# Optimization experiments

Hardware: AMD Instinct MI355X
Metric: run time of the kernel (lower is better)

## Reference

```python
import jax, jax.numpy as jnp
import numpy as np

D_MODEL = 1024
N_HEADS = 16
D_K = D_MODEL // N_HEADS
D_FF = 4096
B, S = 4, 2048
EPS = 1e-5


def setup_inputs() -> dict:
    key = jax.random.key(0)
    ks = jax.random.split(key, 16)
    s = 0.02
    inp = {
        'x': jax.random.normal(ks[0], (B, S, D_MODEL), dtype=jnp.float32),
        'Wq': jax.random.normal(ks[1], (D_MODEL, D_MODEL), dtype=jnp.float32) * s,
        'bq': jnp.zeros((D_MODEL,), jnp.float32),
        'Wk': jax.random.normal(ks[2], (D_MODEL, D_MODEL), dtype=jnp.float32) * s,
        'bk': jnp.zeros((D_MODEL,), jnp.float32),
        'Wv': jax.random.normal(ks[3], (D_MODEL, D_MODEL), dtype=jnp.float32) * s,
        'bv': jnp.zeros((D_MODEL,), jnp.float32),
        'Wo': jax.random.normal(ks[4], (D_MODEL, D_MODEL), dtype=jnp.float32) * s,
        'bo': jnp.zeros((D_MODEL,), jnp.float32),
        'W1': jax.random.normal(ks[5], (D_MODEL, D_FF), dtype=jnp.float32) * s,
        'b1': jnp.zeros((D_FF,), jnp.float32),
        'W2': jax.random.normal(ks[6], (D_FF, D_MODEL), dtype=jnp.float32) * s,
        'b2': jnp.zeros((D_MODEL,), jnp.float32),
        'g1': jnp.ones((D_MODEL,), jnp.float32),
        'be1': jnp.zeros((D_MODEL,), jnp.float32),
        'g2': jnp.ones((D_MODEL,), jnp.float32),
        'be2': jnp.zeros((D_MODEL,), jnp.float32),
    }
    return inp


def _layernorm(x, g, b):
    mu = jnp.mean(x, axis=-1, keepdims=True)
    var = jnp.var(x, axis=-1, keepdims=True)
    return (x - mu) * jax.lax.rsqrt(var + EPS) * g + b


def reference(x, Wq, bq, Wk, bk, Wv, bv, Wo, bo, W1, b1, W2, b2, g1, be1, g2, be2):
    # Multi-head self-attention (mask=None, dropout in eval -> identity)
    q = (x @ Wq + bq).reshape(B, S, N_HEADS, D_K).transpose(0, 2, 1, 3)  # [B,H,S,Dk]
    k = (x @ Wk + bk).reshape(B, S, N_HEADS, D_K).transpose(0, 2, 1, 3)
    v = (x @ Wv + bv).reshape(B, S, N_HEADS, D_K).transpose(0, 2, 1, 3)
    scores = jnp.einsum('bhqd,bhkd->bhqk', q, k) / jnp.sqrt(jnp.float32(D_K))
    attn = jax.nn.softmax(scores, axis=-1)
    out = jnp.einsum('bhqk,bhkd->bhqd', attn, v)          # [B,H,S,Dk]
    out = out.transpose(0, 2, 1, 3).reshape(B, S, D_MODEL)
    att_out = out @ Wo + bo
    x2 = _layernorm(x + att_out, g1, be1)
    ff = jax.nn.relu(x2 @ W1 + b1) @ W2 + b2
    return _layernorm(x2 + ff, g2, be2)
```

## Files before the change

kernel.cpp:

```cpp
#include <hip/hip_runtime.h>
#include <hip/hip_bf16.h>

typedef __attribute__((ext_vector_type(8)))  __bf16 bf16x8;
typedef __attribute__((ext_vector_type(4)))  float  f32x4;
typedef __attribute__((ext_vector_type(16))) float  f32x16;

static __device__ __forceinline__ unsigned short f2bf(float x) {
    unsigned int u = __float_as_uint(x);
    unsigned int r = (u + 0x7FFFu + ((u >> 16) & 1u)) >> 16;
    return (unsigned short)r;
}
static __device__ __forceinline__ float bf2f(unsigned short u) {
    return __uint_as_float(((unsigned int)u) << 16);
}

static __device__ __forceinline__ float fast_exp2(float x) {
    float r;
    asm volatile("v_exp_f32 %0, %1\n\ts_nop 1" : "=v"(r) : "v"(x));
    return r;
}
static __device__ __forceinline__ unsigned int cvt_pk_bf16(float a, float b) {
    unsigned int r;
    asm("v_cvt_pk_bf16_f32 %0, %1, %2" : "=v"(r) : "v"(a), "v"(b));
    return r;
}

static __device__ __forceinline__ void gload_lds16(const ushort* g, ushort* l) {
    __builtin_amdgcn_global_load_lds((const __attribute__((address_space(1))) void*)g,
                                     (__attribute__((address_space(3))) void*)l, 16, 0, 0);
}

static __device__ __forceinline__ int xcd_swz(int id, int nwg) {
    return (id & 7) * (nwg >> 3) + (id >> 3);
}

__global__ __launch_bounds__(256) void cast_bf16_kernel(const float* __restrict__ in,
                                                        ushort* __restrict__ out, int n4) {
    int i = blockIdx.x * 256 + threadIdx.x;
    if (i < n4) {
        float4 v = reinterpret_cast<const float4*>(in)[i];
        ushort4 o;
        o.x = f2bf(v.x); o.y = f2bf(v.y); o.z = f2bf(v.z); o.w = f2bf(v.w);
        reinterpret_cast<ushort4*>(out)[i] = o;
    }
}

__global__ __launch_bounds__(256) void transpose_cast_kernel(const float* __restrict__ in,
                                                             ushort* __restrict__ out,
                                                             int K, int N) {
    __shared__ float tile[32][33];
    const int tx = threadIdx.x;
    const int ty = threadIdx.y;
    const int n0 = blockIdx.x * 32;
    const int k0 = blockIdx.y * 32;
    for (int i = ty; i < 32; i += 8)
        tile[i][tx] = in[(size_t)(k0 + i) * N + n0 + tx];
    __syncthreads();
    for (int i = ty; i < 32; i += 8)
        out[(size_t)(n0 + i) * K + k0 + tx] = f2bf(tile[tx][i]);
}

template<int RELU, int OUTBF, int QKV>
__global__ __launch_bounds__(256) void gemm_db(const ushort* __restrict__ A,
                                               const ushort* __restrict__ Bt,
                                               const float* __restrict__ b0,
                                               const float* __restrict__ b1_,
                                               const float* __restrict__ b2_,
                                               void* __restrict__ Cp,
                                               int M, int N, int K) {
    __shared__ ushort As[2][4096];
    __shared__ ushort Bs[2][4096];
    const int tid  = threadIdx.x;
    const int lane = tid & 63;
    const int w    = tid >> 6;
    const int wr   = w >> 1, wc = w & 1;
    const int nwg = gridDim.x * gridDim.y;
    int wid = xcd_swz(blockIdx.y * gridDim.x + blockIdx.x, nwg);
    const int bx = wid % gridDim.x;
    const int by = wid / gridDim.x;
    const int m0 = by * 128;
    const int n0 = bx * 128;
    const int lr = lane & 15;
    const int lk = (lane >> 4) * 8;

    const int r0 = w * 32 + (lane >> 2);
    const int c8 = (lane & 3) * 8;
    const ushort* gA0 = A  + (size_t)(m0 + r0)      * K + c8;
    const ushort* gA1 = A  + (size_t)(m0 + r0 + 16) * K + c8;
    const ushort* gB0 = Bt + (size_t)(n0 + r0)      * K + c8;
    const ushort* gB1 = Bt + (size_t)(n0 + r0 + 16) * K + c8;
    const int wb = w * 1024;

    f32x4 acc[4][4];
    const f32x4 z = {0.f, 0.f, 0.f, 0.f};
#pragma unroll
    for (int i = 0; i < 4; i++)
#pragma unroll
        for (int j = 0; j < 4; j++) acc[i][j] = z;

    const int nt = K >> 5;

    gload_lds16(gA0, &As[0][wb]);
    gload_lds16(gA1, &As[0][wb + 512]);
    gload_lds16(gB0, &Bs[0][wb]);
    gload_lds16(gB1, &Bs[0][wb + 512]);

    int cur = 0;
    for (int t = 0; t < nt; ++t) {
        __syncthreads();
        if (t + 1 < nt) {
            const int kn = (t + 1) * 32;
            gload_lds16(gA0 + kn, &As[cur ^ 1][wb]);
            gload_lds16(gA1 + kn, &As[cur ^ 1][wb + 512]);
            gload_lds16(gB0 + kn, &Bs[cur ^ 1][wb]);
            gload_lds16(gB1 + kn, &Bs[cur ^ 1][wb + 512]);
        }

        const ushort* Asb = As[cur];
        const ushort* Bsb = Bs[cur];
        bf16x8 af[4], bfr[4];
#pragma unroll
        for (int i = 0; i < 4; i++)
            af[i] = *reinterpret_cast<const bf16x8*>(&Asb[(wr * 64 + i * 16 + lr) * 32 + lk]);
#pragma unroll
        for (int j = 0; j < 4; j++)
            bfr[j] = *reinterpret_cast<const bf16x8*>(&Bsb[(wc * 64 + j * 16 + lr) * 32 + lk]);
#pragma unroll
        for (int i = 0; i < 4; i++)
#pragma unroll
            for (int j = 0; j < 4; j++)
                acc[i][j] = __builtin_amdgcn_mfma_f32_16x16x32_bf16(af[i], bfr[j], acc[i][j], 0, 0, 0);
        cur ^= 1;
    }

    const float* bias;
    float qscale = 1.0f;
    if (QKV) {
        bias = (n0 < 1024) ? b0 : (n0 < 2048 ? b1_ : b2_);
        if (n0 < 1024) qscale = 0.18033688f;
    } else {
        bias = b0;
    }
    const int nb = QKV ? (n0 & 1023) : n0;
    const int rbase = (lane >> 4) * 4;
#pragma unroll
    for (int i = 0; i < 4; i++) {
#pragma unroll
        for (int j = 0; j < 4; j++) {
            const int cloc = wc * 64 + j * 16 + lr;
            const float bv = bias[nb + cloc];
#pragma unroll
            for (int r = 0; r < 4; r++) {
                const int row = m0 + wr * 64 + i * 16 + rbase + r;
                float v = acc[i][j][r] + bv;
                if (RELU) v = v > 0.f ? v : 0.f;
                if (QKV)  v *= qscale;
                if (OUTBF) ((ushort*)Cp)[(size_t)row * N + n0 + cloc] = f2bf(v);
                else       ((float*)Cp)[(size_t)row * N + n0 + cloc] = v;
            }
        }
    }
}

#define ASWZ(row, col) ((row) * 64 + ((col) ^ ((((row) ^ ((row) >> 3)) & 7) << 3)))

__global__ __launch_bounds__(256, 3) void attn_kernel(const ushort* __restrict__ QKV,
                                                      ushort* __restrict__ O) {
    __shared__ ushort Ks[2][4096];
    __shared__ ushort Vt[2][4096];
    const int tid  = threadIdx.x;
    const int lane = tid & 63;
    const int w    = tid >> 6;
    const int l31  = lane & 31;
    const int hi   = lane >> 5;

    int blk = xcd_swz(blockIdx.x, gridDim.x);
    const int qb = blk & 15;
    const int h  = (blk >> 4) & 15;
    const int b  = blk >> 8;
    const int s0 = qb * 128 + w * 32;
    const size_t rowb   = (size_t)b * 2048;
    const size_t base_q = rowb * 3072 + (size_t)h * 64;
    const size_t base_k = base_q + 1024;
    const size_t base_v = base_q + 2048;
    const size_t base_o = rowb * 1024 + (size_t)h * 64;

    bf16x8 qf[4];
#pragma unroll
    for (int ks = 0; ks < 4; ks++)
        qf[ks] = *reinterpret_cast<const bf16x8*>(
            &QKV[base_q + (size_t)(s0 + l31) * 3072 + ks * 16 + 8 * hi]);

    int off8[2][4];
#pragma unroll
    for (int sub = 0; sub < 2; sub++)
#pragma unroll
        for (int ks = 0; ks < 4; ks++)
            off8[sub][ks] = ASWZ(sub * 32 + l31, ks * 16 + 8 * hi);

    const int tS  = tid >> 3;
    const int ccS = tid & 7;
    int vwoff[2][8];
#pragma unroll
    for (int i = 0; i < 2; i++)
#pragma unroll
        for (int jj = 0; jj < 8; jj++)
            vwoff[i][jj] = ASWZ(ccS * 8 + jj, tS + i * 32);
    const int t1  = tS + 32;
    const int sz0 = (tS ^ (tS >> 3)) & 7;
    const int sz1 = (t1 ^ (t1 >> 3)) & 7;
    const ushort* pK0 = QKV + base_k + (size_t)tS * 3072 + (ccS ^ sz0) * 8;
    const ushort* pK1 = QKV + base_k + (size_t)t1 * 3072 + (ccS ^ sz1) * 8;
    const ushort* pV0 = QKV + base_v + (size_t)tS * 3072 + ccS * 8;
    const ushort* pV1 = QKV + base_v + (size_t)t1 * 3072 + ccS * 8;
    const size_t step = (size_t)64 * 3072;

    gload_lds16(pK0, &Ks[0][w * 512]);
    gload_lds16(pK1, &Ks[0][2048 + w * 512]);
    {
        int4 v0 = *reinterpret_cast<const int4*>(pV0);
        int4 v1 = *reinterpret_cast<const int4*>(pV1);
        const ushort* vs0 = reinterpret_cast<const ushort*>(&v0);
        const ushort* vs1 = reinterpret_cast<const ushort*>(&v1);
#pragma unroll
        for (int jj = 0; jj < 8; jj++) Vt[0][vwoff[0][jj]] = vs0[jj];
#pragma unroll
        for (int jj = 0; jj < 8; jj++) Vt[0][vwoff[1][jj]] = vs1[jj];
    }
    pK0 += step; pK1 += step; pV0 += step; pV1 += step;
    __syncthreads();

    f32x16 oacc0, oacc1;
    for (int i = 0; i < 16; i++) { oacc0[i] = 0.f; oacc1[i] = 0.f; }
    float lacc = 0.f;
    int cur = 0;

    for (int it = 0; it < 32; ++it) {
        int4 nv0, nv1;
        if (it < 31) {
            gload_lds16(pK0, &Ks[cur ^ 1][w * 512]);
            gload_lds16(pK1, &Ks[cur ^ 1][2048 + w * 512]);
            nv0 = *reinterpret_cast<const int4*>(pV0);
            nv1 = *reinterpret_cast<const int4*>(pV1);
            pK0 += step; pK1 += step; pV0 += step; pV1 += step;
        }

        f32x16 sa0, sa1;
        for (int i = 0; i < 16; i++) { sa0[i] = 0.f; sa1[i] = 0.f; }
        __builtin_amdgcn_s_setprio(1);
#pragma unroll
        for (int ks = 0; ks < 4; ks++) {
            bf16x8 k0 = *reinterpret_cast<const bf16x8*>(&Ks[cur][off8[0][ks]]);
            sa0 = __builtin_amdgcn_mfma_f32_32x32x16_bf16(k0, qf[ks], sa0, 0, 0, 0);
        }
#pragma unroll
        for (int ks = 0; ks < 4; ks++) {
            bf16x8 k1 = *reinterpret_cast<const bf16x8*>(&Ks[cur][off8[1][ks]]);
            sa1 = __builtin_amdgcn_mfma_f32_32x32x16_bf16(k1, qf[ks], sa1, 0, 0, 0);
        }
        __builtin_amdgcn_s_setprio(0);

        unsigned pk0[8], pk1[8];
#pragma unroll
        for (int i = 0; i < 8; i++) {
            float plo = fast_exp2(sa0[2 * i]);
            float phi = fast_exp2(sa0[2 * i + 1]);
            lacc += plo + phi;
            pk0[i] = cvt_pk_bf16(plo, phi);
        }
#pragma unroll
        for (int i = 0; i < 8; i++) {
            float plo = fast_exp2(sa1[2 * i]);
            float phi = fast_exp2(sa1[2 * i + 1]);
            lacc += plo + phi;
            pk1[i] = cvt_pk_bf16(plo, phi);
        }

        __builtin_amdgcn_s_setprio(1);
#pragma unroll
        for (int ks = 0; ks < 4; ks++) {
            const int bi = 4 * (ks & 1);
            unsigned a, bb, c, d;
            if (ks < 2) { a = pk0[bi]; bb = pk0[bi + 1]; c = pk0[bi + 2]; d = pk0[bi + 3]; }
            else        { a = pk1[bi]; bb = pk1[bi + 1]; c = pk1[bi + 2]; d = pk1[bi + 3]; }
            asm("v_permlane32_swap_b32 %0, %1" : "+v"(a), "+v"(c));
            asm("v_permlane32_swap_b32 %0, %1" : "+v"(bb), "+v"(d));
            union { unsigned u[4]; bf16x8 v; } fr;
            fr.u[0] = a; fr.u[1] = bb; fr.u[2] = c; fr.u[3] = d;
            bf16x8 v0 = *reinterpret_cast<const bf16x8*>(&Vt[cur][off8[0][ks]]);
            oacc0 = __builtin_amdgcn_mfma_f32_32x32x16_bf16(fr.v, v0, oacc0, 0, 0, 0);
            bf16x8 v1 = *reinterpret_cast<const bf16x8*>(&Vt[cur][off8[1][ks]]);
            oacc1 = __builtin_amdgcn_mfma_f32_32x32x16_bf16(fr.v, v1, oacc1, 0, 0, 0);
        }
        __builtin_amdgcn_s_setprio(0);

        if (it < 31) {
            const ushort* vs0 = reinterpret_cast<const ushort*>(&nv0);
            const ushort* vs1 = reinterpret_cast<const ushort*>(&nv1);
#pragma unroll
            for (int jj = 0; jj < 8; jj++) Vt[cur ^ 1][vwoff[0][jj]] = vs0[jj];
#pragma unroll
            for (int jj = 0; jj < 8; jj++) Vt[cur ^ 1][vwoff[1][jj]] = vs1[jj];
        }
        __syncthreads();
        cur ^= 1;
    }

    const float ltot = lacc + __shfl_xor(lacc, 32);
    const float inv  = 1.f / ltot;
#pragma unroll
    for (int r = 0; r < 16; r++) {
        const int qloc = (r & 3) + 8 * (r >> 2) + 4 * hi;
        const float invq = __shfl(inv, qloc);
        const size_t rowoff = base_o + (size_t)(s0 + qloc) * 1024 + l31;
        O[rowoff]      = f2bf(oacc0[r] * invq);
        O[rowoff + 32] = f2bf(oacc1[r] * invq);
    }
}

__global__ __launch_bounds__(256) void ln_res_fb(const float* __restrict__ x,
                                                 const ushort* __restrict__ y,
                                                 const float* __restrict__ g,
                                                 const float* __restrict__ be,
                                                 ushort* __restrict__ outb) {
    const int row = blockIdx.x;
    const int tid = threadIdx.x;
    const float4 xv = reinterpret_cast<const float4*>(x + (size_t)row * 1024)[tid];
    const ushort4 yv = reinterpret_cast<const ushort4*>(y + (size_t)row * 1024)[tid];
    float v[4] = {xv.x + bf2f(yv.x), xv.y + bf2f(yv.y), xv.z + bf2f(yv.z), xv.w + bf2f(yv.w)};
    float s  = v[0] + v[1] + v[2] + v[3];
    float s2 = v[0]*v[0] + v[1]*v[1] + v[2]*v[2] + v[3]*v[3];
    for (int off = 32; off; off >>= 1) { s += __shfl_down(s, off); s2 += __shfl_down(s2, off); }
    __shared__ float red[8];
    const int w = tid >> 6, lane = tid & 63;
    if (lane == 0) { red[w] = s; red[4 + w] = s2; }
    __syncthreads();
    if (tid == 0) {
        const float ts  = red[0] + red[1] + red[2] + red[3];
        const float ts2 = red[4] + red[5] + red[6] + red[7];
        const float mu  = ts * (1.f / 1024.f);
        const float var = ts2 * (1.f / 1024.f) - mu * mu;
        red[0] = mu;
        red[1] = rsqrtf(var + 1e-5f);
    }
    __syncthreads();
    const float mu = red[0], rs = red[1];
    const float4 gv = reinterpret_cast<const float4*>(g)[tid];
    const float4 bv = reinterpret_cast<const float4*>(be)[tid];
    ushort4 ob;
    ob.x = f2bf((v[0] - mu) * rs * gv.x + bv.x);
    ob.y = f2bf((v[1] - mu) * rs * gv.y + bv.y);
    ob.z = f2bf((v[2] - mu) * rs * gv.z + bv.z);
    ob.w = f2bf((v[3] - mu) * rs * gv.w + bv.w);
    reinterpret_cast<ushort4*>(outb + (size_t)row * 1024)[tid] = ob;
}

__global__ __launch_bounds__(256) void ln_res_bb(const ushort* __restrict__ x,
                                                 const ushort* __restrict__ y,
                                                 const float* __restrict__ g,
                                                 const float* __restrict__ be,
                                                 float* __restrict__ outf) {
    const int row = blockIdx.x;
    const int tid = threadIdx.x;
    const ushort4 xv = reinterpret_cast<const ushort4*>(x + (size_t)row * 1024)[tid];
    const ushort4 yv = reinterpret_cast<const ushort4*>(y + (size_t)row * 1024)[tid];
    float v[4] = {bf2f(xv.x) + bf2f(yv.x), bf2f(xv.y) + bf2f(yv.y),
                  bf2f(xv.z) + bf2f(yv.z), bf2f(xv.w) + bf2f(yv.w)};
    float s  = v[0] + v[1] + v[2] + v[3];
    float s2 = v[0]*v[0] + v[1]*v[1] + v[2]*v[2] + v[3]*v[3];
    for (int off = 32; off; off >>= 1) { s += __shfl_down(s, off); s2 += __shfl_down(s2, off); }
    __shared__ float red[8];
    const int w = tid >> 6, lane = tid & 63;
    if (lane == 0) { red[w] = s; red[4 + w] = s2; }
    __syncthreads();
    if (tid == 0) {
        const float ts  = red[0] + red[1] + red[2] + red[3];
        const float ts2 = red[4] + red[5] + red[6] + red[7];
        const float mu  = ts * (1.f / 1024.f);
        const float var = ts2 * (1.f / 1024.f) - mu * mu;
        red[0] = mu;
        red[1] = rsqrtf(var + 1e-5f);
    }
    __syncthreads();
    const float mu = red[0], rs = red[1];
    const float4 gv = reinterpret_cast<const float4*>(g)[tid];
    const float4 bv = reinterpret_cast<const float4*>(be)[tid];
    float4 of;
    of.x = (v[0] - mu) * rs * gv.x + bv.x;
    of.y = (v[1] - mu) * rs * gv.y + bv.y;
    of.z = (v[2] - mu) * rs * gv.z + bv.z;
    of.w = (v[3] - mu) * rs * gv.w + bv.w;
    reinterpret_cast<float4*>(outf + (size_t)row * 1024)[tid] = of;
}

extern "C" void kernel_launch(void* const* d_in, const int* in_sizes, int n_in,
                              void* d_out, int out_size, void* d_ws, size_t ws_size,
                              hipStream_t stream) {
    const float* x  = (const float*)d_in[0];
    const float* Wq = (const float*)d_in[1];  const float* bq = (const float*)d_in[2];
    const float* Wk = (const float*)d_in[3];  const float* bk = (const float*)d_in[4];
    const float* Wv = (const float*)d_in[5];  const float* bv = (const float*)d_in[6];
    const float* Wo = (const float*)d_in[7];  const float* bo = (const float*)d_in[8];
    const float* W1 = (const float*)d_in[9];  const float* b1 = (const float*)d_in[10];
    const float* W2 = (const float*)d_in[11]; const float* b2 = (const float*)d_in[12];
    const float* g1 = (const float*)d_in[13]; const float* be1 = (const float*)d_in[14];
    const float* g2 = (const float*)d_in[15]; const float* be2 = (const float*)d_in[16];

    char* ws = (char*)d_ws;
    const size_t MBy = (size_t)1 << 20;
    ushort* xb    = (ushort*)(ws + 0 * MBy);
    ushort* wqkvT = (ushort*)(ws + 16 * MBy);
    ushort* woT   = (ushort*)(ws + 22 * MBy);
    ushort* w1T   = (ushort*)(ws + 24 * MBy);
    ushort* w2T   = (ushort*)(ws + 32 * MBy);
    ushort* QKVb  = (ushort*)(ws + 40 * MBy);
    ushort* AOb   = (ushort*)(ws + 88 * MBy);
    ushort* h1    = (ushort*)(ws + 40 * MBy);
    ushort* y1b   = (ushort*)(ws + 104 * MBy);
    ushort* y2b   = (ushort*)(ws + 104 * MBy);
    ushort* x2b   = (ushort*)(ws + 120 * MBy);
    (void)ws_size; (void)n_in; (void)in_sizes; (void)out_size;

    const int M = 8192;

    cast_bf16_kernel<<<(M * 1024 / 4 + 255) / 256, 256, 0, stream>>>(x, xb, M * 1024 / 4);
    dim3 tb(32, 8);
    transpose_cast_kernel<<<dim3(32, 32),  tb, 0, stream>>>(Wq, wqkvT,               1024, 1024);
    transpose_cast_kernel<<<dim3(32, 32),  tb, 0, stream>>>(Wk, wqkvT + 1024 * 1024, 1024, 1024);
    transpose_cast_kernel<<<dim3(32, 32),  tb, 0, stream>>>(Wv, wqkvT + 2048 * 1024, 1024, 1024);
    transpose_cast_kernel<<<dim3(32, 32),  tb, 0, stream>>>(Wo, woT, 1024, 1024);
    transpose_cast_kernel<<<dim3(128, 32), tb, 0, stream>>>(W1, w1T, 1024, 4096);
    transpose_cast_kernel<<<dim3(32, 128), tb, 0, stream>>>(W2, w2T, 4096, 1024);

    gemm_db<0, 1, 1><<<dim3(24, 64), 256, 0, stream>>>(xb, wqkvT, bq, bk, bv, QKVb,
                                                       M, 3072, 1024);

    attn_kernel<<<1024, 256, 0, stream>>>(QKVb, AOb);

    gemm_db<0, 1, 0><<<dim3(8, 64), 256, 0, stream>>>(AOb, woT, bo, nullptr, nullptr, y1b,
                                                      M, 1024, 1024);

    ln_res_fb<<<M, 256, 0, stream>>>(x, y1b, g1, be1, x2b);

    gemm_db<1, 1, 0><<<dim3(32, 64), 256, 0, stream>>>(x2b, w1T, b1, nullptr, nullptr, h1,
                                                       M, 4096, 1024);
    gemm_db<0, 1, 0><<<dim3(8, 64), 256, 0, stream>>>(h1, w2T, b2, nullptr, nullptr, y2b,
                                                      M, 1024, 4096);

    ln_res_bb<<<M, 256, 0, stream>>>(x2b, y2b, g2, be2, (float*)d_out);
}
```

Baseline: 430.9 us.

## Triple-buffer GEMM LDS pipeline with explicit vmcnt waits, merge QKV weight transposes

The GEMM now keeps three LDS stages and prefetches two K-tiles ahead. It replaces the blanket __syncthreads with a partial s_waitcnt vmcnt(4) plus a bare barrier, so global loads can overlap more MFMA work. The three Q/K/V weight transpose launches are also merged into one 3D-grid launch to cut launch overhead. LDS use per block rises from 32KB to 48KB, which may lower occupancy. The explicit wait counts also depend on the compiler not issuing other vector memory ops in the loop.

```diff
diff --git a/kernel.cpp b/kernel.cpp
--- a/kernel.cpp
+++ b/kernel.cpp
@@ -28,6 +28,12 @@
 static __device__ __forceinline__ void gload_lds16(const ushort* g, ushort* l) {
     __builtin_amdgcn_global_load_lds((const __attribute__((address_space(1))) void*)g,
                                      (__attribute__((address_space(3))) void*)l, 16, 0, 0);
+}
+
+static __device__ __forceinline__ void barrier_fence() {
+    __builtin_amdgcn_s_barrier();
+    __builtin_amdgcn_sched_barrier(0);
+    asm volatile("" ::: "memory");
 }
 
 static __device__ __forceinline__ int xcd_swz(int id, int nwg) {
@@ -60,16 +66,35 @@
         out[(size_t)(n0 + i) * K + k0 + tx] = f2bf(tile[tx][i]);
 }
 
+__global__ __launch_bounds__(256) void transpose_cast3_kernel(const float* __restrict__ w0,
+                                                              const float* __restrict__ w1,
+                                                              const float* __restrict__ w2,
+                                                              ushort* __restrict__ out) {
+    __shared__ float tile[32][33];
+    const int tx = threadIdx.x;
+    const int ty = threadIdx.y;
+    const int n0 = blockIdx.x * 32;
+    const int k0 = blockIdx.y * 32;
+    const int z  = blockIdx.z;
+    const float* in = (z == 0) ? w0 : (z == 1 ? w1 : w2);
+    ushort* o = out + (size_t)z * 1024 * 1024;
+    for (int i = ty; i < 32; i += 8)
+        tile[i][tx] = in[(size_t)(k0 + i) * 1024 + n0 + tx];
+    __syncthreads();
+    for (int i = ty; i < 32; i += 8)
+        o[(size_t)(n0 + i) * 1024 + k0 + tx] = f2bf(tile[tx][i]);
+}
+
 template<int RELU, int OUTBF, int QKV>
-__global__ __launch_bounds__(256) void gemm_db(const ushort* __restrict__ A,
+__global__ __launch_bounds__(256) void gemm_p3(const ushort* __restrict__ A,
                                                const ushort* __restrict__ Bt,
                                                const float* __restrict__ b0,
                                                const float* __restrict__ b1_,
                                                const float* __restrict__ b2_,
                                                void* __restrict__ Cp,
                                                int M, int N, int K) {
-    __shared__ ushort As[2][4096];
-    __shared__ ushort Bs[2][4096];
+    __shared__ ushort As[3][4096];
+    __shared__ ushort Bs[3][4096];
     const int tid  = threadIdx.x;
     const int lane = tid & 63;
     const int w    = tid >> 6;
@@ -100,20 +125,28 @@
 
     const int nt = K >> 5;
 
-    gload_lds16(gA0, &As[0][wb]);
-    gload_lds16(gA1, &As[0][wb + 512]);
-    gload_lds16(gB0, &Bs[0][wb]);
-    gload_lds16(gB1, &Bs[0][wb + 512]);
+#pragma unroll
+    for (int t = 0; t < 2; ++t) {
+        const int kn = t * 32;
+        gload_lds16(gA0 + kn, &As[t][wb]);
+        gload_lds16(gA1 + kn, &As[t][wb + 512]);
+        gload_lds16(gB0 + kn, &Bs[t][wb]);
+        gload_lds16(gB1 + kn, &Bs[t][wb + 512]);
+    }
 
     int cur = 0;
     for (int t = 0; t < nt; ++t) {
-        __syncthreads();
-        if (t + 1 < nt) {
-            const int kn = (t + 1) * 32;
-            gload_lds16(gA0 + kn, &As[cur ^ 1][wb]);
-            gload_lds16(gA1 + kn, &As[cur ^ 1][wb + 512]);
-            gload_lds16(gB0 + kn, &Bs[cur ^ 1][wb]);
-            gload_lds16(gB1 + kn, &Bs[cur ^ 1][wb + 512]);
+        if (t + 1 < nt) asm volatile("s_waitcnt vmcnt(4)" ::: "memory");
+        else            asm volatile("s_waitcnt vmcnt(0)" ::: "memory");
+        barrier_fence();
+
+        if (t + 2 < nt) {
+            const int bi = (cur + 2 >= 3) ? cur - 1 : cur + 2;
+            const int kn = (t + 2) * 32;
+            gload_lds16(gA0 + kn, &As[bi][wb]);
+            gload_lds16(gA1 + kn, &As[bi][wb + 512]);
+            gload_lds16(gB0 + kn, &Bs[bi][wb]);
+            gload_lds16(gB1 + kn, &Bs[bi][wb + 512]);
         }
 
         const ushort* Asb = As[cur];
@@ -130,7 +163,8 @@
 #pragma unroll
             for (int j = 0; j < 4; j++)
                 acc[i][j] = __builtin_amdgcn_mfma_f32_16x16x32_bf16(af[i], bfr[j], acc[i][j], 0, 0, 0);
-        cur ^= 1;
+
+        cur = (cur == 2) ? 0 : cur + 1;
     }
 
     const float* bias;
@@ -425,26 +459,24 @@
 
     cast_bf16_kernel<<<(M * 1024 / 4 + 255) / 256, 256, 0, stream>>>(x, xb, M * 1024 / 4);
     dim3 tb(32, 8);
-    transpose_cast_kernel<<<dim3(32, 32),  tb, 0, stream>>>(Wq, wqkvT,               1024, 1024);
-    transpose_cast_kernel<<<dim3(32, 32),  tb, 0, stream>>>(Wk, wqkvT + 1024 * 1024, 1024, 1024);
-    transpose_cast_kernel<<<dim3(32, 32),  tb, 0, stream>>>(Wv, wqkvT + 2048 * 1024, 1024, 1024);
+    transpose_cast3_kernel<<<dim3(32, 32, 3), tb, 0, stream>>>(Wq, Wk, Wv, wqkvT);
     transpose_cast_kernel<<<dim3(32, 32),  tb, 0, stream>>>(Wo, woT, 1024, 1024);
     transpose_cast_kernel<<<dim3(128, 32), tb, 0, stream>>>(W1, w1T, 1024, 4096);
     transpose_cast_kernel<<<dim3(32, 128), tb, 0, stream>>>(W2, w2T, 4096, 1024);
 
-    gemm_db<0, 1, 1><<<dim3(24, 64), 256, 0, stream>>>(xb, wqkvT, bq, bk, bv, QKVb,
+    gemm_p3<0, 1, 1><<<dim3(24, 64), 256, 0, stream>>>(xb, wqkvT, bq, bk, bv, QKVb,
                                                        M, 3072, 1024);
 
     attn_kernel<<<1024, 256, 0, stream>>>(QKVb, AOb);
 
-    gemm_db<0, 1, 0><<<dim3(8, 64), 256, 0, stream>>>(AOb, woT, bo, nullptr, nullptr, y1b,
+    gemm_p3<0, 1, 0><<<dim3(8, 64), 256, 0, stream>>>(AOb, woT, bo, nullptr, nullptr, y1b,
                                                       M, 1024, 1024);
 
     ln_res_fb<<<M, 256, 0, stream>>>(x, y1b, g1, be1, x2b);
 
-    gemm_db<1, 1, 0><<<dim3(32, 64), 256, 0, stream>>>(x2b, w1T, b1, nullptr, nullptr, h1,
+    gemm_p3<1, 1, 0><<<dim3(32, 64), 256, 0, stream>>>(x2b, w1T, b1, nullptr, nullptr, h1,
                                                        M, 4096, 1024);
-    gemm_db<0, 1, 0><<<dim3(8, 64), 256, 0, stream>>>(h1, w2T, b2, nullptr, nullptr, y2b,
+    gemm_p3<0, 1, 0><<<dim3(8, 64), 256, 0, stream>>>(h1, w2T, b2, nullptr, nullptr, y2b,
                                                       M, 1024, 4096);
 
     ln_res_bb<<<M, 256, 0, stream>>>(x2b, y2b, g2, be2, (float*)d_out);
```

Measured after the change: 428.7 us. About the same (-0.5%).
